# Kernel tuning notes

Measured on AMD Instinct MI355X. Metric: run time of the kernel, lower is better.

## Reference

```python
import jax, jax.numpy as jnp
import numpy as np


def setup_inputs() -> dict:
    key = jax.random.key(0)
    k1, k2 = jax.random.split(key)
    B, N, M = 4, 16384, 4096
    src_points = jax.random.normal(k1, (B, N, 3), dtype=jnp.float32)
    target_verts = jax.random.normal(k2, (B, M, 3), dtype=jnp.float32)
    return {"src_points": src_points, "target_verts": target_verts}


def reference(src_points, target_verts):
    # target_faces=None path of ChamferLoss: degenerate one-vertex triangles,
    # so closest-point-on-mesh == nearest target vertex.
    # d2[b,n,m] = ||p_bn - v_bm||^2 via the expansion p2 + v2 - 2 p.v
    p2 = jnp.sum(src_points * src_points, axis=-1)          # (B, N)
    v2 = jnp.sum(target_verts * target_verts, axis=-1)      # (B, M)
    pv = jnp.einsum('bnd,bmd->bnm', src_points, target_verts)  # (B, N, M)
    d2 = p2[:, :, None] + v2[:, None, :] - 2.0 * pv
    d2 = jnp.maximum(d2, 0.0)
    min_d2 = jnp.min(d2, axis=-1)                            # (B, N)
    num_src_per_batch = src_points.shape[1]
    loss = jnp.sum(min_d2, axis=-1) / num_src_per_batch      # (B,)
    return loss
```

## Files before the change

### kernel.cpp

```cpp
#include <hip/hip_runtime.h>
#include <float.h>


typedef __bf16 bf16x8 __attribute__((ext_vector_type(8)));
typedef float  f32x16 __attribute__((ext_vector_type(16)));

constexpr int B = 4, N = 16384, M = 4096;
constexpr int BN = B * N;
constexpr int NCHUNK = 8;
constexpr int CHUNK_V = M / NCHUNK;
constexpr int TILES = CHUNK_V / 32;
constexpr int TPB = 256;
constexpr int PPB = 128;
constexpr int PBLK = BN / PPB;
constexpr size_t BFRAG_BYTES = (size_t)B * M * 32;

__global__ __launch_bounds__(256) void chamfer_pre(
    const float* __restrict__ tv, unsigned char* __restrict__ bfr,
    float* __restrict__ out)
{
    if (blockIdx.x == 0 && threadIdx.x < B) out[threadIdx.x] = 0.0f;
    int i = blockIdx.x * 256 + threadIdx.x;
    int m = i & (M - 1);
    float x = tv[3 * i + 0], y = tv[3 * i + 1], z = tv[3 * i + 2];
    __bf16 xh = (__bf16)x, yh = (__bf16)y, zh = (__bf16)z;
    float xhf = (float)xh, yhf = (float)yh, zhf = (float)zh;
    __bf16 xl = (__bf16)(x - xhf), yl = (__bf16)(y - yhf), zl = (__bf16)(z - zhf);
    float v2 = fmaf(x, x, fmaf(y, y, z * z));
    __bf16 v2h = (__bf16)v2;
    __bf16 v2l = (__bf16)(v2 - (float)v2h);
    __bf16 zero = (__bf16)0.0f;

    bf16x8 h0, h1;
    h0[0] = (__bf16)(-2.0f * xhf); h0[1] = (__bf16)(-2.0f * yhf);
    h0[2] = (__bf16)(-2.0f * zhf);
    h0[3] = h0[0]; h0[4] = h0[1]; h0[5] = h0[2];
    h0[6] = (__bf16)(-2.0f * (float)xl); h0[7] = (__bf16)(-2.0f * (float)yl);
    h1[0] = (__bf16)(-2.0f * (float)zl); h1[1] = v2h; h1[2] = v2l;
    h1[3] = zero; h1[4] = zero; h1[5] = zero; h1[6] = zero; h1[7] = zero;

    int chunk = m >> 9, local = m & (CHUNK_V - 1), tile = local >> 5, r = m & 31;
    size_t base = (size_t)(i >> 12) * 131072 + (size_t)chunk * 16384
                + tile * 1024 + r * 16;
    *(bf16x8*)(bfr + base)       = h0;
    *(bf16x8*)(bfr + base + 512) = h1;
}

__global__ __launch_bounds__(TPB) void chamfer_mfma(
    const float* __restrict__ src, const unsigned char* __restrict__ bfr,
    float* __restrict__ partial)
{
    __shared__ uint4 lds4[1024];
    const char* ldsc = (const char*)lds4;
    const int blk   = blockIdx.x;
    const int chunk = blk & 7;
    const int pblk  = blk >> 3;
    const int b     = pblk >> 7;
    const int t     = threadIdx.x;
    const int w     = t >> 6, L = t & 63;
    const int half  = L >> 5, c = L & 31;

    const uint4* gsrc = (const uint4*)(bfr + (size_t)b * 131072 + (size_t)chunk * 16384);
#pragma unroll
    for (int i = 0; i < 4; ++i) lds4[i * 256 + t] = gsrc[i * 256 + t];

    const int gp = pblk * PPB + w * 32 + c;
    float ax = src[3 * gp], ay = src[3 * gp + 1], az = src[3 * gp + 2];
    float pp = fmaf(ax, ax, fmaf(ay, ay, az * az));
    __bf16 one = (__bf16)1.0f, zero = (__bf16)0.0f;
    bf16x8 bP;
    {
        __bf16 xh = (__bf16)ax, yh = (__bf16)ay, zh = (__bf16)az;
        __bf16 xl = (__bf16)(ax - (float)xh), yl = (__bf16)(ay - (float)yh),
               zl = (__bf16)(az - (float)zh);
        if (half == 0) { bP[0]=xh; bP[1]=yh; bP[2]=zh; bP[3]=xl; bP[4]=yl; bP[5]=zl; bP[6]=xh; bP[7]=yh; }
        else { bP[0]=zh; bP[1]=one; bP[2]=one; bP[3]=zero; bP[4]=zero; bP[5]=zero; bP[6]=zero; bP[7]=zero; }
    }

    float mn[8];
    f32x16 zeroC;
#pragma unroll
    for (int u = 0; u < 8; ++u) mn[u] = FLT_MAX;
#pragma unroll
    for (int r = 0; r < 16; ++r) zeroC[r] = 0.0f;

    __syncthreads();

    const int laneoff = half * 512 + c * 16;
#pragma unroll 4
    for (int tl = 0; tl < TILES; ++tl) {
        bf16x8 av = *(const bf16x8*)(ldsc + tl * 1024 + laneoff);
        f32x16 C = __builtin_amdgcn_mfma_f32_32x32x16_bf16(av, bP, zeroC, 0, 0, 0);
#pragma unroll
        for (int u = 0; u < 8; ++u)
            mn[u] = fminf(fminf(mn[u], C[2 * u]), C[2 * u + 1]);
    }

    float m01 = fminf(fminf(mn[0], mn[1]), fminf(mn[2], mn[3]));
    float m23 = fminf(fminf(mn[4], mn[5]), fminf(mn[6], mn[7]));
    float m = fminf(m01, m23);
    m = fminf(m, __shfl_xor(m, 32, 64));
    if (L < 32)
        partial[(size_t)chunk * BN + gp] = m + pp;
}

__global__ __launch_bounds__(256) void chamfer_reduce(
    const float* __restrict__ partial, float* __restrict__ out)
{
    const int p = blockIdx.x * 256 + threadIdx.x;
    const int b = blockIdx.x >> 6;
    float m = FLT_MAX;
#pragma unroll
    for (int cgr = 0; cgr < NCHUNK; ++cgr)
        m = fminf(m, partial[(size_t)cgr * BN + p]);
    float sum = fmaxf(m, 0.0f);

    for (int off = 32; off > 0; off >>= 1)
        sum += __shfl_down(sum, off, 64);
    __shared__ float acc[4];
    if ((threadIdx.x & 63) == 0) acc[threadIdx.x >> 6] = sum;
    __syncthreads();
    if (threadIdx.x == 0) {
        float s = acc[0] + acc[1] + acc[2] + acc[3];
        atomicAdd(&out[b], s * (1.0f / N));
    }
}

extern "C" void kernel_launch(void* const* d_in, const int* in_sizes, int n_in,
                              void* d_out, int out_size, void* d_ws, size_t ws_size,
                              hipStream_t stream) {
    const float* src = (const float*)d_in[0];
    const float* tv  = (const float*)d_in[1];
    float* out = (float*)d_out;
    unsigned char* bfr = (unsigned char*)d_ws;
    float* partial = (float*)((char*)d_ws + BFRAG_BYTES);

    chamfer_pre   <<<(B * M) / 256, 256, 0, stream>>>(tv, bfr, out);
    chamfer_mfma  <<<PBLK * NCHUNK, TPB, 0, stream>>>(src, bfr, partial);
    chamfer_reduce<<<BN / 256, 256, 0, stream>>>(partial, out);
}
```

Baseline: 75.17 us.

## Register-tile vertex and point fragments, drop LDS staging, precompute point fragments

The MFMA kernel no longer stages vertex fragments through LDS. Each wave loads 8 vertex tiles directly into registers and reuses them across 4 point groups, and point bf16 fragments plus squared norms are precomputed in the pre kernel. The vertex dimension is split into 16 chunks instead of 8, and the point norm is added in the reduce step. This aims to cut LDS traffic and syncs and raise the MFMA-to-load ratio. In exchange it doubles the partial buffer written and read by the reduce and adds extra prepass work.

```diff
diff --git a/kernel.cpp b/kernel.cpp
--- a/kernel.cpp
+++ b/kernel.cpp
@@ -7,113 +7,130 @@
 
 constexpr int B = 4, N = 16384, M = 4096;
 constexpr int BN = B * N;
-constexpr int NCHUNK = 8;
-constexpr int CHUNK_V = M / NCHUNK;
-constexpr int TILES = CHUNK_V / 32;
+constexpr int VT = 8;
+constexpr int NVC = M / (VT * 32);
+constexpr int G = 4;
 constexpr int TPB = 256;
-constexpr int PPB = 128;
-constexpr int PBLK = BN / PPB;
-constexpr size_t BFRAG_BYTES = (size_t)B * M * 32;
+constexpr int PPB = 4 * G * 32;
+constexpr int NPB = BN / PPB;
+
+constexpr size_t VFRAG_BYTES = (size_t)B * M * 32;
+constexpr size_t PFRAG_BYTES = (size_t)BN * 32;
+constexpr size_t PP_BYTES    = (size_t)BN * 4;
 
 __global__ __launch_bounds__(256) void chamfer_pre(
-    const float* __restrict__ tv, unsigned char* __restrict__ bfr,
-    float* __restrict__ out)
+    const float* __restrict__ src, const float* __restrict__ tv,
+    unsigned char* __restrict__ vfr, unsigned char* __restrict__ pfr,
+    float* __restrict__ pp, float* __restrict__ out)
 {
     if (blockIdx.x == 0 && threadIdx.x < B) out[threadIdx.x] = 0.0f;
-    int i = blockIdx.x * 256 + threadIdx.x;
-    int m = i & (M - 1);
-    float x = tv[3 * i + 0], y = tv[3 * i + 1], z = tv[3 * i + 2];
-    __bf16 xh = (__bf16)x, yh = (__bf16)y, zh = (__bf16)z;
-    float xhf = (float)xh, yhf = (float)yh, zhf = (float)zh;
-    __bf16 xl = (__bf16)(x - xhf), yl = (__bf16)(y - yhf), zl = (__bf16)(z - zhf);
-    float v2 = fmaf(x, x, fmaf(y, y, z * z));
-    __bf16 v2h = (__bf16)v2;
-    __bf16 v2l = (__bf16)(v2 - (float)v2h);
-    __bf16 zero = (__bf16)0.0f;
+    __bf16 one = (__bf16)1.0f, zero = (__bf16)0.0f;
 
-    bf16x8 h0, h1;
-    h0[0] = (__bf16)(-2.0f * xhf); h0[1] = (__bf16)(-2.0f * yhf);
-    h0[2] = (__bf16)(-2.0f * zhf);
-    h0[3] = h0[0]; h0[4] = h0[1]; h0[5] = h0[2];
-    h0[6] = (__bf16)(-2.0f * (float)xl); h0[7] = (__bf16)(-2.0f * (float)yl);
-    h1[0] = (__bf16)(-2.0f * (float)zl); h1[1] = v2h; h1[2] = v2l;
-    h1[3] = zero; h1[4] = zero; h1[5] = zero; h1[6] = zero; h1[7] = zero;
+    if (blockIdx.x < (B * M) / 256) {
+        int i = blockIdx.x * 256 + threadIdx.x;
+        float x = tv[3 * i + 0], y = tv[3 * i + 1], z = tv[3 * i + 2];
+        __bf16 xh = (__bf16)x, yh = (__bf16)y, zh = (__bf16)z;
+        float xhf = (float)xh, yhf = (float)yh, zhf = (float)zh;
+        __bf16 xl = (__bf16)(x - xhf), yl = (__bf16)(y - yhf), zl = (__bf16)(z - zhf);
+        float v2 = fmaf(x, x, fmaf(y, y, z * z));
+        __bf16 v2h = (__bf16)v2;
+        __bf16 v2l = (__bf16)(v2 - (float)v2h);
 
-    int chunk = m >> 9, local = m & (CHUNK_V - 1), tile = local >> 5, r = m & 31;
-    size_t base = (size_t)(i >> 12) * 131072 + (size_t)chunk * 16384
-                + tile * 1024 + r * 16;
-    *(bf16x8*)(bfr + base)       = h0;
-    *(bf16x8*)(bfr + base + 512) = h1;
+        bf16x8 h0, h1;
+        h0[0] = (__bf16)(-2.0f * xhf); h0[1] = (__bf16)(-2.0f * yhf);
+        h0[2] = (__bf16)(-2.0f * zhf);
+        h0[3] = h0[0]; h0[4] = h0[1]; h0[5] = h0[2];
+        h0[6] = (__bf16)(-2.0f * (float)xl); h0[7] = (__bf16)(-2.0f * (float)yl);
+        h1[0] = (__bf16)(-2.0f * (float)zl); h1[1] = v2h; h1[2] = v2l;
+        h1[3] = zero; h1[4] = zero; h1[5] = zero; h1[6] = zero; h1[7] = zero;
+
+        int m = i & (M - 1);
+        size_t base = (size_t)(i >> 12) * 131072 + (size_t)(m >> 5) * 1024
+                    + (size_t)(m & 31) * 16;
+        *(bf16x8*)(vfr + base)       = h0;
+        *(bf16x8*)(vfr + base + 512) = h1;
+    } else {
+        int i = (blockIdx.x - (B * M) / 256) * 256 + threadIdx.x;
+        float x = src[3 * i + 0], y = src[3 * i + 1], z = src[3 * i + 2];
+        __bf16 xh = (__bf16)x, yh = (__bf16)y, zh = (__bf16)z;
+        __bf16 xl = (__bf16)(x - (float)xh), yl = (__bf16)(y - (float)yh),
+               zl = (__bf16)(z - (float)zh);
+        bf16x8 h0, h1;
+        h0[0] = xh; h0[1] = yh; h0[2] = zh; h0[3] = xl;
+        h0[4] = yl; h0[5] = zl; h0[6] = xh; h0[7] = yh;
+        h1[0] = zh; h1[1] = one; h1[2] = one; h1[3] = zero;
+        h1[4] = zero; h1[5] = zero; h1[6] = zero; h1[7] = zero;
+
+        size_t base = (size_t)(i >> 5) * 1024 + (size_t)(i & 31) * 16;
+        *(bf16x8*)(pfr + base)       = h0;
+        *(bf16x8*)(pfr + base + 512) = h1;
+        pp[i] = fmaf(x, x, fmaf(y, y, z * z));
+    }
 }
 
 __global__ __launch_bounds__(TPB) void chamfer_mfma(
-    const float* __restrict__ src, const unsigned char* __restrict__ bfr,
+    const unsigned char* __restrict__ vfr, const unsigned char* __restrict__ pfr,
     float* __restrict__ partial)
 {
-    __shared__ uint4 lds4[1024];
-    const char* ldsc = (const char*)lds4;
-    const int blk   = blockIdx.x;
-    const int chunk = blk & 7;
-    const int pblk  = blk >> 3;
-    const int b     = pblk >> 7;
-    const int t     = threadIdx.x;
-    const int w     = t >> 6, L = t & 63;
-    const int half  = L >> 5, c = L & 31;
+    const int blk  = blockIdx.x;
+    const int vc   = blk & (NVC - 1);
+    const int pblk = blk >> 4;
+    const int b    = pblk >> 5;
+    const int t    = threadIdx.x;
+    const int w    = t >> 6, L = t & 63;
+    const int half = L >> 5, c = L & 31;
+    const int laneoff = half * 512 + c * 16;
 
-    const uint4* gsrc = (const uint4*)(bfr + (size_t)b * 131072 + (size_t)chunk * 16384);
+    const unsigned char* abase =
+        vfr + (size_t)b * 131072 + (size_t)vc * (VT * 1024) + laneoff;
+    bf16x8 av[VT];
 #pragma unroll
-    for (int i = 0; i < 4; ++i) lds4[i * 256 + t] = gsrc[i * 256 + t];
+    for (int tt = 0; tt < VT; ++tt)
+        av[tt] = *(const bf16x8*)(abase + tt * 1024);
 
-    const int gp = pblk * PPB + w * 32 + c;
-    float ax = src[3 * gp], ay = src[3 * gp + 1], az = src[3 * gp + 2];
-    float pp = fmaf(ax, ax, fmaf(ay, ay, az * az));
-    __bf16 one = (__bf16)1.0f, zero = (__bf16)0.0f;
-    bf16x8 bP;
-    {
-        __bf16 xh = (__bf16)ax, yh = (__bf16)ay, zh = (__bf16)az;
-        __bf16 xl = (__bf16)(ax - (float)xh), yl = (__bf16)(ay - (float)yh),
-               zl = (__bf16)(az - (float)zh);
-        if (half == 0) { bP[0]=xh; bP[1]=yh; bP[2]=zh; bP[3]=xl; bP[4]=yl; bP[5]=zl; bP[6]=xh; bP[7]=yh; }
-        else { bP[0]=zh; bP[1]=one; bP[2]=one; bP[3]=zero; bP[4]=zero; bP[5]=zero; bP[6]=zero; bP[7]=zero; }
-    }
+    const int pg0 = pblk * (PPB / 32) + w * G;
+    bf16x8 bP[G];
+#pragma unroll
+    for (int g = 0; g < G; ++g)
+        bP[g] = *(const bf16x8*)(pfr + (size_t)(pg0 + g) * 1024 + laneoff);
 
-    float mn[8];
     f32x16 zeroC;
-#pragma unroll
-    for (int u = 0; u < 8; ++u) mn[u] = FLT_MAX;
 #pragma unroll
     for (int r = 0; r < 16; ++r) zeroC[r] = 0.0f;
 
-    __syncthreads();
-
-    const int laneoff = half * 512 + c * 16;
-#pragma unroll 4
-    for (int tl = 0; tl < TILES; ++tl) {
-        bf16x8 av = *(const bf16x8*)(ldsc + tl * 1024 + laneoff);
-        f32x16 C = __builtin_amdgcn_mfma_f32_32x32x16_bf16(av, bP, zeroC, 0, 0, 0);
 #pragma unroll
-        for (int u = 0; u < 8; ++u)
-            mn[u] = fminf(fminf(mn[u], C[2 * u]), C[2 * u + 1]);
+    for (int g = 0; g < G; ++g) {
+        float mn[8];
+#pragma unroll
+        for (int u = 0; u < 8; ++u) mn[u] = FLT_MAX;
+#pragma unroll
+        for (int tt = 0; tt < VT; ++tt) {
+            f32x16 C = __builtin_amdgcn_mfma_f32_32x32x16_bf16(
+                av[tt], bP[g], zeroC, 0, 0, 0);
+#pragma unroll
+            for (int u = 0; u < 8; ++u)
+                mn[u] = fminf(fminf(mn[u], C[2 * u]), C[2 * u + 1]);
+        }
+        float m01 = fminf(fminf(mn[0], mn[1]), fminf(mn[2], mn[3]));
+        float m23 = fminf(fminf(mn[4], mn[5]), fminf(mn[6], mn[7]));
+        float m = fminf(m01, m23);
+        m = fminf(m, __shfl_xor(m, 32, 64));
+        if (L < 32)
+            partial[(size_t)vc * BN + (size_t)(pg0 + g) * 32 + c] = m;
     }
-
-    float m01 = fminf(fminf(mn[0], mn[1]), fminf(mn[2], mn[3]));
-    float m23 = fminf(fminf(mn[4], mn[5]), fminf(mn[6], mn[7]));
-    float m = fminf(m01, m23);
-    m = fminf(m, __shfl_xor(m, 32, 64));
-    if (L < 32)
-        partial[(size_t)chunk * BN + gp] = m + pp;
 }
 
 __global__ __launch_bounds__(256) void chamfer_reduce(
-    const float* __restrict__ partial, float* __restrict__ out)
+    const float* __restrict__ partial, const float* __restrict__ pp,
+    float* __restrict__ out)
 {
     const int p = blockIdx.x * 256 + threadIdx.x;
     const int b = blockIdx.x >> 6;
     float m = FLT_MAX;
 #pragma unroll
-    for (int cgr = 0; cgr < NCHUNK; ++cgr)
-        m = fminf(m, partial[(size_t)cgr * BN + p]);
-    float sum = fmaxf(m, 0.0f);
+    for (int vc = 0; vc < NVC; ++vc)
+        m = fminf(m, partial[(size_t)vc * BN + p]);
+    float sum = fmaxf(m + pp[p], 0.0f);
 
     for (int off = 32; off > 0; off >>= 1)
         sum += __shfl_down(sum, off, 64);
@@ -132,10 +149,13 @@
     const float* src = (const float*)d_in[0];
     const float* tv  = (const float*)d_in[1];
     float* out = (float*)d_out;
-    unsigned char* bfr = (unsigned char*)d_ws;
-    float* partial = (float*)((char*)d_ws + BFRAG_BYTES);
 
-    chamfer_pre   <<<(B * M) / 256, 256, 0, stream>>>(tv, bfr, out);
-    chamfer_mfma  <<<PBLK * NCHUNK, TPB, 0, stream>>>(src, bfr, partial);
-    chamfer_reduce<<<BN / 256, 256, 0, stream>>>(partial, out);
+    unsigned char* vfr = (unsigned char*)d_ws;
+    unsigned char* pfr = vfr + VFRAG_BYTES;
+    float* pp          = (float*)(pfr + PFRAG_BYTES);
+    float* partial     = (float*)((char*)pp + PP_BYTES);
+
+    chamfer_pre   <<<(B * M) / 256 + BN / 256, 256, 0, stream>>>(src, tv, vfr, pfr, pp, out);
+    chamfer_mfma  <<<NVC * NPB, TPB, 0, stream>>>(vfr, pfr, partial);
+    chamfer_reduce<<<BN / 256, 256, 0, stream>>>(partial, pp, out);
 }
```

Result: slower. 77.73 us (+3.4%).
